# Kernel optimization log

Hardware: AMD Instinct MI355X
Metric: run time of the kernel (lower is better)

Reference implementation:

```python
import jax, jax.numpy as jnp
import numpy as np

B, D, H = 32768, 1024, 16
HD = D // H  # head_dim = 64
EPS = 1e-5


def setup_inputs() -> dict:
    key = jax.random.key(0)
    ks = jax.random.split(key, 12)
    s = 1.0 / np.sqrt(D)
    return {
        "sa_hidden": jax.random.normal(ks[0], (B, D), jnp.float32),
        "state_hidden": jax.random.normal(ks[1], (B, D), jnp.float32),
        "Wq": jax.random.normal(ks[2], (D, D), jnp.float32) * s,
        "bq": jax.random.normal(ks[3], (D,), jnp.float32) * s,
        "Wk": jax.random.normal(ks[4], (D, D), jnp.float32) * s,
        "bk": jax.random.normal(ks[5], (D,), jnp.float32) * s,
        "Wv": jax.random.normal(ks[6], (D, D), jnp.float32) * s,
        "bv": jax.random.normal(ks[7], (D,), jnp.float32) * s,
        "Wo": jax.random.normal(ks[8], (D, D), jnp.float32) * s,
        "bo": jax.random.normal(ks[9], (D,), jnp.float32) * s,
        "ln_w": jnp.ones((D,), jnp.float32),
        "ln_b": jnp.zeros((D,), jnp.float32),
    }


def reference(sa_hidden, state_hidden, Wq, bq, Wk, bk, Wv, bv, Wo, bo, ln_w, ln_b):
    b = sa_hidden.shape[0]
    # QKV projections (torch Linear: x @ W.T + b)
    Q = (sa_hidden @ Wq.T + bq).reshape(b, H, HD)
    K = (state_hidden @ Wk.T + bk).reshape(b, H, HD)
    V = (state_hidden @ Wv.T + bv).reshape(b, H, HD)
    # head-wise attention: [b, H, H] scores over the heads axis
    energy = jnp.einsum("bhd,bgd->bhg", Q, K) / np.sqrt(HD).astype(np.float32)
    attn = jax.nn.softmax(energy, axis=-1)
    out = jnp.einsum("bhg,bgd->bhd", attn, V)  # [b, H, HD]
    # transpose(1,2).view(b, D): flatten in (head_dim, heads) order
    out = jnp.swapaxes(out, 1, 2).reshape(b, D)
    out = out @ Wo.T + bo
    # residual + LayerNorm
    x = out + sa_hidden
    mu = jnp.mean(x, axis=-1, keepdims=True)
    var = jnp.mean((x - mu) ** 2, axis=-1, keepdims=True)
    return (x - mu) * jax.lax.rsqrt(var + EPS) * ln_w + ln_b
```

## Files before the change

### kernel.cpp

```cpp
#include <hip/hip_runtime.h>

typedef unsigned int  uint32;
typedef float  f32x4   __attribute__((ext_vector_type(4)));
typedef __bf16 bf16x8  __attribute__((ext_vector_type(8)));
typedef short  s16x4   __attribute__((ext_vector_type(4)));

__device__ __forceinline__ float bf2f(unsigned int u) {
  return __builtin_bit_cast(float, u << 16);
}
__device__ __forceinline__ unsigned short f2bf(float f) {
  uint32 u = __builtin_bit_cast(uint32, f);
  u += 0x7fffu + ((u >> 16) & 1u);
  return (unsigned short)(u >> 16);
}

__device__ __forceinline__ void gload_lds16(const void* g, void* l) {
  __builtin_amdgcn_global_load_lds(
      (const __attribute__((address_space(1))) void*)g,
      (__attribute__((address_space(3))) void*)l, 16, 0, 0);
}

__global__ __launch_bounds__(256) void cast_kernel(
    const float* __restrict__ x, unsigned short* __restrict__ y, int n8) {
  int i = blockIdx.x * 256 + threadIdx.x;
  if (i >= n8) return;
  const float4* xp = (const float4*)x;
  float4 a = xp[2 * i], b = xp[2 * i + 1];
  uint4 o;
  o.x = (uint32)f2bf(a.x) | ((uint32)f2bf(a.y) << 16);
  o.y = (uint32)f2bf(a.z) | ((uint32)f2bf(a.w) << 16);
  o.z = (uint32)f2bf(b.x) | ((uint32)f2bf(b.y) << 16);
  o.w = (uint32)f2bf(b.z) | ((uint32)f2bf(b.w) << 16);
  ((uint4*)y)[i] = o;
}

__global__ __launch_bounds__(256) void cat2_kernel(
    const float* __restrict__ a, const float* __restrict__ b,
    float* __restrict__ o) {
  int i = blockIdx.x * 256 + threadIdx.x;
  o[i] = (i < 1024) ? a[i] : b[i - 1024];
}

template <int EPI>
__global__ __launch_bounds__(512, 2) void gemm256(
    const unsigned short* __restrict__ A, const unsigned short* __restrict__ W,
    const float* __restrict__ bias, const float* __restrict__ resid,
    unsigned short* __restrict__ Ob, float* __restrict__ Of,
    int M, int N, int K) {
  __shared__ char smem[131072];
  const int tid  = threadIdx.x;
  const int lane = tid & 63;
  const int wave = tid >> 6;
  const int wr   = wave >> 2;
  const int wc   = wave & 3;

  const int nwg = gridDim.x;
  const int xcd = blockIdx.x & 7;
  const int r   = blockIdx.x >> 3;
  const int NT  = N >> 8;
  const int m0  = (xcd * ((nwg >> 3) / NT) + r / NT) << 8;
  const int n0  = (r % NT) << 8;

  f32x4 acc[8][4];
#pragma unroll
  for (int m = 0; m < 8; ++m)
#pragma unroll
    for (int n = 0; n < 4; ++n) acc[m][n] = (f32x4)0.0f;

  const int pr8 = lane >> 3;
  const int cl  = (lane & 7) ^ pr8;
  const int rA0 = (wave * 2) * 16 + pr8 * 2 + (cl >> 2);
  const int kb8 = (cl & 3) * 8;
  const unsigned short* As0 = A + (size_t)(m0 + rA0) * K + kb8;
  const unsigned short* As1 = As0 + (size_t)16 * K;
  const unsigned short* Bs0 = W + (size_t)(n0 + rA0) * K + kb8;
  const unsigned short* Bs1 = Bs0 + (size_t)16 * K;
  const int dA = wave * 2048 + lane * 16;

#define STAGE(d, kt)                                                          \
  {                                                                           \
    char* sb = smem + (d) * 32768;                                            \
    const int ko = (kt) * 32;                                                 \
    gload_lds16(As0 + ko, sb + dA);                                           \
    gload_lds16(As1 + ko, sb + dA + 1024);                                    \
    gload_lds16(Bs0 + ko, sb + 16384 + dA);                                   \
    gload_lds16(Bs1 + ko, sb + 16384 + dA + 1024);                            \
  }

  const int fr  = lane & 15, kg = lane >> 4, frh = fr >> 1;
  const int cA  = ((((fr & 1) * 4) + kg) ^ frh) * 16;
  const int aoff = (wr * 64 + frh) * 128 + cA;
  const int boff = 16384 + (wc * 32 + frh) * 128 + cA;

#define MFMAS(base_)                                                          \
  {                                                                           \
    bf16x8 av[8], bv[4];                                                      \
    _Pragma("unroll") for (int m = 0; m < 8; ++m)                             \
        av[m] = *(const bf16x8*)((base_) + aoff + m * 1024);                  \
    _Pragma("unroll") for (int n = 0; n < 4; ++n)                             \
        bv[n] = *(const bf16x8*)((base_) + boff + n * 1024);                  \
    __builtin_amdgcn_s_setprio(1);                                            \
    _Pragma("unroll") for (int m = 0; m < 8; ++m)                             \
        _Pragma("unroll") for (int n = 0; n < 4; ++n)                         \
            acc[m][n] = __builtin_amdgcn_mfma_f32_16x16x32_bf16(              \
                av[m], bv[n], acc[m][n], 0, 0, 0);                            \
    __builtin_amdgcn_s_setprio(0);                                            \
  }

  const int nt = K >> 5;
  STAGE(0, 0);
  STAGE(1, 1);
  STAGE(2, 2);

  for (int t = 0; t < nt - 3; ++t) {
    asm volatile("s_waitcnt vmcnt(8)" ::: "memory");
    __builtin_amdgcn_s_barrier();
    const char* base = smem + (t & 3) * 32768;
    bf16x8 av[8], bv[4];
#pragma unroll
    for (int m = 0; m < 8; ++m)
      av[m] = *(const bf16x8*)(base + aoff + m * 1024);
#pragma unroll
    for (int n = 0; n < 4; ++n)
      bv[n] = *(const bf16x8*)(base + boff + n * 1024);
    STAGE((t + 3) & 3, t + 3);
    __builtin_amdgcn_s_setprio(1);
#pragma unroll
    for (int m = 0; m < 8; ++m)
#pragma unroll
      for (int n = 0; n < 4; ++n)
        acc[m][n] = __builtin_amdgcn_mfma_f32_16x16x32_bf16(av[m], bv[n],
                                                            acc[m][n], 0, 0, 0);
    __builtin_amdgcn_s_setprio(0);
    asm volatile("s_waitcnt lgkmcnt(0)" ::: "memory");
    __builtin_amdgcn_s_barrier();
  }
  asm volatile("s_waitcnt vmcnt(8)" ::: "memory");
  __builtin_amdgcn_s_barrier();
  MFMAS(smem + ((nt - 3) & 3) * 32768);
  asm volatile("s_waitcnt vmcnt(4)" ::: "memory");
  __builtin_amdgcn_s_barrier();
  MFMAS(smem + ((nt - 2) & 3) * 32768);
  asm volatile("s_waitcnt vmcnt(0)" ::: "memory");
  __builtin_amdgcn_s_barrier();
  MFMAS(smem + ((nt - 1) & 3) * 32768);

  const int r4 = (lane >> 4) * 4;
#pragma unroll
  for (int n = 0; n < 4; ++n) {
    const int col = n0 + wc * 64 + n * 16 + fr;
    const float bvv = bias[col];
#pragma unroll
    for (int m = 0; m < 8; ++m) {
      const int row = m0 + wr * 128 + m * 16 + r4;
#pragma unroll
      for (int i = 0; i < 4; ++i) {
        const size_t idx = (size_t)(row + i) * N + col;
        float v = acc[m][n][i] + bvv;
        if constexpr (EPI == 0) {
          Ob[idx] = f2bf(v);
        } else {
          Of[idx] = v + resid[idx];
        }
      }
    }
  }
#undef STAGE
#undef MFMAS
}

__global__ __launch_bounds__(256) void attn_kernel(
    const unsigned short* __restrict__ Q, const unsigned short* __restrict__ KV,
    unsigned short* __restrict__ O) {
  const int tid  = threadIdx.x;
  const int lane = tid & 63;
  const int wave = tid >> 6;
  const int b    = blockIdx.x * 4 + wave;
  const size_t qb  = (size_t)b * 1024;
  const size_t kvb = (size_t)b * 2048;
  const int fr = lane & 15, kg = lane >> 4;

  const bf16x8 kf0 = *(const bf16x8*)(KV + kvb + fr * 64 + kg * 8);
  const bf16x8 kf1 = *(const bf16x8*)(KV + kvb + fr * 64 + 32 + kg * 8);
  const bf16x8 qf0 = *(const bf16x8*)(Q + qb + fr * 64 + kg * 8);
  const bf16x8 qf1 = *(const bf16x8*)(Q + qb + fr * 64 + 32 + kg * 8);

  s16x4 vb[4];
#pragma unroll
  for (int c = 0; c < 4; ++c) {
    const unsigned short* vp = KV + kvb + 1024 + c * 16 + fr + kg * 4 * 64;
    s16x4 t;
    t[0] = (short)vp[0];
    t[1] = (short)vp[64];
    t[2] = (short)vp[128];
    t[3] = (short)vp[192];
    vb[c] = t;
  }

  f32x4 es = (f32x4)0.0f;
  es = __builtin_amdgcn_mfma_f32_16x16x32_bf16(kf0, qf0, es, 0, 0, 0);
  es = __builtin_amdgcn_mfma_f32_16x16x32_bf16(kf1, qf1, es, 0, 0, 0);

  float s0 = es[0] * 0.125f, s1 = es[1] * 0.125f;
  float s2 = es[2] * 0.125f, s3 = es[3] * 0.125f;
  float mx = fmaxf(fmaxf(s0, s1), fmaxf(s2, s3));
  mx = fmaxf(mx, __shfl_xor(mx, 16, 64));
  mx = fmaxf(mx, __shfl_xor(mx, 32, 64));
  float e0 = __expf(s0 - mx), e1 = __expf(s1 - mx);
  float e2 = __expf(s2 - mx), e3 = __expf(s3 - mx);
  float sum = e0 + e1 + e2 + e3;
  sum += __shfl_xor(sum, 16, 64);
  sum += __shfl_xor(sum, 32, 64);
  const float inv = 1.0f / sum;

  s16x4 pa;
  pa[0] = (short)f2bf(e0 * inv);
  pa[1] = (short)f2bf(e1 * inv);
  pa[2] = (short)f2bf(e2 * inv);
  pa[3] = (short)f2bf(e3 * inv);

  unsigned short* Ob = O + qb;
#pragma unroll
  for (int c = 0; c < 4; ++c) {
    f32x4 o = __builtin_amdgcn_mfma_f32_16x16x16bf16_1k(pa, vb[c],
                                                        (f32x4)0.0f, 0, 0, 0);
    uint2 st;
    st.x = (uint32)f2bf(o[0]) | ((uint32)f2bf(o[1]) << 16);
    st.y = (uint32)f2bf(o[2]) | ((uint32)f2bf(o[3]) << 16);
    *(uint2*)(Ob + c * 256 + fr * 16 + kg * 4) = st;
  }
}

__global__ __launch_bounds__(256) void ln_kernel(
    float* __restrict__ Y, const float* __restrict__ gw,
    const float* __restrict__ gb) {
  float* y = Y + (size_t)blockIdx.x * 1024;
  const int tid = threadIdx.x;
  float4 v = ((const float4*)y)[tid];
  float s  = v.x + v.y + v.z + v.w;
  float s2 = v.x * v.x + v.y * v.y + v.z * v.z + v.w * v.w;
#pragma unroll
  for (int o = 32; o > 0; o >>= 1) {
    s  += __shfl_xor(s, o, 64);
    s2 += __shfl_xor(s2, o, 64);
  }
  __shared__ float rs[4], rq[4];
  const int wave = tid >> 6;
  if ((tid & 63) == 0) { rs[wave] = s; rq[wave] = s2; }
  __syncthreads();
  s  = rs[0] + rs[1] + rs[2] + rs[3];
  s2 = rq[0] + rq[1] + rq[2] + rq[3];
  const float mean = s * (1.f / 1024.f);
  const float var  = s2 * (1.f / 1024.f) - mean * mean;
  const float r = rsqrtf(var + 1e-5f);
  const float4 w = ((const float4*)gw)[tid];
  const float4 bb = ((const float4*)gb)[tid];
  float4 o;
  o.x = (v.x - mean) * r * w.x + bb.x;
  o.y = (v.y - mean) * r * w.y + bb.y;
  o.z = (v.z - mean) * r * w.z + bb.z;
  o.w = (v.w - mean) * r * w.w + bb.w;
  ((float4*)y)[tid] = o;
}

extern "C" void kernel_launch(void* const* d_in, const int* in_sizes, int n_in,
                              void* d_out, int out_size, void* d_ws,
                              size_t ws_size, hipStream_t stream) {
  const float* sa = (const float*)d_in[0];
  const float* st = (const float*)d_in[1];
  const float* Wq = (const float*)d_in[2];
  const float* bq = (const float*)d_in[3];
  const float* Wk = (const float*)d_in[4];
  const float* bk = (const float*)d_in[5];
  const float* Wv = (const float*)d_in[6];
  const float* bv = (const float*)d_in[7];
  const float* Wo = (const float*)d_in[8];
  const float* bo = (const float*)d_in[9];
  const float* lw = (const float*)d_in[10];
  const float* lb = (const float*)d_in[11];
  float* out = (float*)d_out;

  const int M = 32768, D = 1024;
  const size_t MiB = 1024 * 1024;
  char* w = (char*)d_ws;
  unsigned short* saB  = (unsigned short*)(w);
  unsigned short* stB  = (unsigned short*)(w + 64 * MiB);
  unsigned short* WqB  = (unsigned short*)(w + 128 * MiB);
  unsigned short* WkvB = (unsigned short*)(w + 130 * MiB);
  unsigned short* WoB  = (unsigned short*)(w + 134 * MiB);
  unsigned short* Qb   = (unsigned short*)(w + 136 * MiB);
  float* bkv = (float*)(w + 128 * MiB);
  unsigned short* KVb = (unsigned short*)d_out;
  unsigned short* attb = saB;

  const int nH8 = M * D / 8;
  const int nW8 = D * D / 8;
  cast_kernel<<<nH8 / 256, 256, 0, stream>>>(sa, saB, nH8);
  cast_kernel<<<nH8 / 256, 256, 0, stream>>>(st, stB, nH8);
  cast_kernel<<<nW8 / 256, 256, 0, stream>>>(Wq, WqB, nW8);
  cast_kernel<<<nW8 / 256, 256, 0, stream>>>(Wk, (unsigned short*)WkvB, nW8);
  cast_kernel<<<nW8 / 256, 256, 0, stream>>>(Wv, (unsigned short*)WkvB + D * D, nW8);
  cast_kernel<<<nW8 / 256, 256, 0, stream>>>(Wo, WoB, nW8);

  gemm256<0><<<(M / 256) * (D / 256), 512, 0, stream>>>(
      saB, WqB, bq, nullptr, Qb, nullptr, M, D, D);

  cat2_kernel<<<8, 256, 0, stream>>>(bk, bv, bkv);
  gemm256<0><<<(M / 256) * (2 * D / 256), 512, 0, stream>>>(
      stB, WkvB, bkv, nullptr, KVb, nullptr, M, 2 * D, D);

  attn_kernel<<<M / 4, 256, 0, stream>>>(Qb, KVb, attb);

  gemm256<1><<<(M / 256) * (D / 256), 512, 0, stream>>>(
      attb, WoB, bo, sa, nullptr, out, M, D, D);

  ln_kernel<<<M, 256, 0, stream>>>(out, lw, lb);
}
```

Measured before the change: 558.9 us.

## Restructure GEMM main loop to BK=64 double-buffered LDS with interleaved MFMA phases

Switches the bf16 GEMM from a 4-stage, K-step-32 LDS pipeline to a 2-stage pipeline with K-step 64. It uses a new XOR-swizzled LDS layout and splits each tile's MFMAs into four phases, interleaving LDS fragment reads with MFMA issue. The next stage's global-to-LDS loads are issued before the last MFMA phase to overlap memory with compute. The aim is fewer barriers per K and better hiding of LDS read latency. The cost is 128KB of LDS per block, which may limit occupancy, and a shallower prefetch depth.

```diff
diff --git a/kernel.cpp b/kernel.cpp
--- a/kernel.cpp
+++ b/kernel.cpp
@@ -69,94 +69,106 @@
 
   const int pr8 = lane >> 3;
   const int cl  = (lane & 7) ^ pr8;
-  const int rA0 = (wave * 2) * 16 + pr8 * 2 + (cl >> 2);
-  const int kb8 = (cl & 3) * 8;
-  const unsigned short* As0 = A + (size_t)(m0 + rA0) * K + kb8;
-  const unsigned short* As1 = As0 + (size_t)16 * K;
-  const unsigned short* Bs0 = W + (size_t)(n0 + rA0) * K + kb8;
-  const unsigned short* Bs1 = Bs0 + (size_t)16 * K;
-  const int dA = wave * 2048 + lane * 16;
+  const unsigned short* As = A + (size_t)(m0 + wave * 8 + pr8) * K + cl * 8;
+  const unsigned short* Bs = W + (size_t)(n0 + wave * 8 + pr8) * K + cl * 8;
+  const int dst = wave * 1024 + lane * 16;
 
 #define STAGE(d, kt)                                                          \
   {                                                                           \
-    char* sb = smem + (d) * 32768;                                            \
-    const int ko = (kt) * 32;                                                 \
-    gload_lds16(As0 + ko, sb + dA);                                           \
-    gload_lds16(As1 + ko, sb + dA + 1024);                                    \
-    gload_lds16(Bs0 + ko, sb + 16384 + dA);                                   \
-    gload_lds16(Bs1 + ko, sb + 16384 + dA + 1024);                            \
-  }
-
-  const int fr  = lane & 15, kg = lane >> 4, frh = fr >> 1;
-  const int cA  = ((((fr & 1) * 4) + kg) ^ frh) * 16;
-  const int aoff = (wr * 64 + frh) * 128 + cA;
-  const int boff = 16384 + (wc * 32 + frh) * 128 + cA;
-
-#define MFMAS(base_)                                                          \
+    char* sb = smem + (d) * 65536;                                            \
+    const int ko = (kt) * 64;                                                 \
+    _Pragma("unroll") for (int j = 0; j < 4; ++j)                             \
+        gload_lds16(As + (size_t)(j * 64) * K + ko, sb + j * 8192 + dst);     \
+    _Pragma("unroll") for (int j = 0; j < 4; ++j)                             \
+        gload_lds16(Bs + (size_t)(j * 64) * K + ko,                           \
+                    sb + 32768 + j * 8192 + dst);                             \
+  }
+
+  const int fr = lane & 15, kg = lane >> 4;
+  int cA[2];
+#pragma unroll
+  for (int ks = 0; ks < 2; ++ks)
+    cA[ks] = fr * 128 + (((ks * 4 + kg) ^ (fr & 7)) * 16);
+  const int abase = wr * 16384;
+  const int bbase = 32768 + wc * 8192;
+
+#define PH_AB(base_, av_, bv_, mlo, ks)                                       \
   {                                                                           \
-    bf16x8 av[8], bv[4];                                                      \
-    _Pragma("unroll") for (int m = 0; m < 8; ++m)                             \
-        av[m] = *(const bf16x8*)((base_) + aoff + m * 1024);                  \
+    _Pragma("unroll") for (int m = 0; m < 4; ++m)                             \
+        av_[m] = *(const bf16x8*)((base_) + abase + ((mlo) + m) * 2048 +      \
+                                  cA[ks]);                                    \
     _Pragma("unroll") for (int n = 0; n < 4; ++n)                             \
-        bv[n] = *(const bf16x8*)((base_) + boff + n * 1024);                  \
-    __builtin_amdgcn_s_setprio(1);                                            \
-    _Pragma("unroll") for (int m = 0; m < 8; ++m)                             \
-        _Pragma("unroll") for (int n = 0; n < 4; ++n)                         \
-            acc[m][n] = __builtin_amdgcn_mfma_f32_16x16x32_bf16(              \
-                av[m], bv[n], acc[m][n], 0, 0, 0);                            \
-    __builtin_amdgcn_s_setprio(0);                                            \
-  }
-
-  const int nt = K >> 5;
+        bv_[n] = *(const bf16x8*)((base_) + bbase + n * 2048 + cA[ks]);       \
+  }
+#define PH_A(base_, av_, mlo, ks)                                             \
+  {                                                                           \
+    _Pragma("unroll") for (int m = 0; m < 4; ++m)                             \
+        av_[m] = *(const bf16x8*)((base_) + abase + ((mlo) + m) * 2048 +      \
+                                  cA[ks]);                                    \
+  }
+#define PH_MFMA(av_, bv_, mlo)                                                \
+  __builtin_amdgcn_s_setprio(1);                                              \
+  _Pragma("unroll") for (int m = 0; m < 4; ++m)                               \
+      _Pragma("unroll") for (int n = 0; n < 4; ++n)                           \
+          acc[(mlo) + m][n] = __builtin_amdgcn_mfma_f32_16x16x32_bf16(        \
+              av_[m], bv_[n], acc[(mlo) + m][n], 0, 0, 0);                    \
+  __builtin_amdgcn_s_setprio(0);
+
+  const int nt = K >> 6;
   STAGE(0, 0);
   STAGE(1, 1);
-  STAGE(2, 2);
-
-  for (int t = 0; t < nt - 3; ++t) {
+
+  for (int t = 0; t < nt - 2; ++t) {
     asm volatile("s_waitcnt vmcnt(8)" ::: "memory");
     __builtin_amdgcn_s_barrier();
-    const char* base = smem + (t & 3) * 32768;
-    bf16x8 av[8], bv[4];
-#pragma unroll
-    for (int m = 0; m < 8; ++m)
-      av[m] = *(const bf16x8*)(base + aoff + m * 1024);
-#pragma unroll
-    for (int n = 0; n < 4; ++n)
-      bv[n] = *(const bf16x8*)(base + boff + n * 1024);
-    STAGE((t + 3) & 3, t + 3);
-    __builtin_amdgcn_s_setprio(1);
-#pragma unroll
-    for (int m = 0; m < 8; ++m)
-#pragma unroll
-      for (int n = 0; n < 4; ++n)
-        acc[m][n] = __builtin_amdgcn_mfma_f32_16x16x32_bf16(av[m], bv[n],
-                                                            acc[m][n], 0, 0, 0);
-    __builtin_amdgcn_s_setprio(0);
+    const char* base = smem + (t & 1) * 65536;
+    bf16x8 a0[4], a1[4], b0[4], b1[4];
+    PH_AB(base, a0, b0, 0, 0);
+    PH_MFMA(a0, b0, 0);
+    PH_A(base, a1, 4, 0);
+    PH_MFMA(a1, b0, 4);
+    PH_AB(base, a0, b1, 0, 1);
+    PH_MFMA(a0, b1, 0);
+    PH_A(base, a1, 4, 1);
     asm volatile("s_waitcnt lgkmcnt(0)" ::: "memory");
     __builtin_amdgcn_s_barrier();
-  }
-  asm volatile("s_waitcnt vmcnt(8)" ::: "memory");
-  __builtin_amdgcn_s_barrier();
-  MFMAS(smem + ((nt - 3) & 3) * 32768);
-  asm volatile("s_waitcnt vmcnt(4)" ::: "memory");
-  __builtin_amdgcn_s_barrier();
-  MFMAS(smem + ((nt - 2) & 3) * 32768);
-  asm volatile("s_waitcnt vmcnt(0)" ::: "memory");
-  __builtin_amdgcn_s_barrier();
-  MFMAS(smem + ((nt - 1) & 3) * 32768);
+    STAGE(t & 1, t + 2);
+    __builtin_amdgcn_sched_barrier(0);
+    PH_MFMA(a1, b1, 4);
+  }
+#pragma unroll
+  for (int tt = 0; tt < 2; ++tt) {
+    if (tt == 0)
+      asm volatile("s_waitcnt vmcnt(8)" ::: "memory");
+    else
+      asm volatile("s_waitcnt vmcnt(0)" ::: "memory");
+    __builtin_amdgcn_s_barrier();
+    const char* base = smem + ((nt - 2 + tt) & 1) * 65536;
+    bf16x8 a0[4], a1[4], b0[4], b1[4];
+    PH_AB(base, a0, b0, 0, 0);
+    PH_MFMA(a0, b0, 0);
+    PH_A(base, a1, 4, 0);
+    PH_MFMA(a1, b0, 4);
+    PH_AB(base, a0, b1, 0, 1);
+    PH_MFMA(a0, b1, 0);
+    PH_A(base, a1, 4, 1);
+    PH_MFMA(a1, b1, 4);
+  }
 
   const int r4 = (lane >> 4) * 4;
-#pragma unroll
-  for (int n = 0; n < 4; ++n) {
-    const int col = n0 + wc * 64 + n * 16 + fr;
-    const float bvv = bias[col];
-#pragma unroll
-    for (int m = 0; m < 8; ++m) {
-      const int row = m0 + wr * 128 + m * 16 + r4;
-#pragma unroll
-      for (int i = 0; i < 4; ++i) {
-        const size_t idx = (size_t)(row + i) * N + col;
-        float v = acc[m][n][i] + bvv;
+  float bvv[4];
+#pragma unroll
+  for (int n = 0; n < 4; ++n) bvv[n] = bias[n0 + wc * 64 + n * 16 + fr];
+#pragma unroll
+  for (int m = 0; m < 8; ++m) {
+    const int rowb = m0 + wr * 128 + m * 16 + r4;
+#pragma unroll
+    for (int i = 0; i < 4; ++i) {
+      const size_t rb = (size_t)(rowb + i) * N;
+#pragma unroll
+      for (int n = 0; n < 4; ++n) {
+        const size_t idx = rb + (n0 + wc * 64 + n * 16 + fr);
+        float v = acc[m][n][i] + bvv[n];
         if constexpr (EPI == 0) {
           Ob[idx] = f2bf(v);
         } else {
@@ -166,7 +178,9 @@
     }
   }
 #undef STAGE
-#undef MFMAS
+#undef PH_AB
+#undef PH_A
+#undef PH_MFMA
 }
 
 __global__ __launch_bounds__(256) void attn_kernel(
```

Measured after the change: 501.6 us. -10.2%, faster.
